# Kernel optimization log

Measured on AMD Instinct MI355X. Metric: run time of the kernel, lower is better.

## Reference

```python
import jax, jax.numpy as jnp
import numpy as np

LSTM = 512
N = 2048   # memory_size
D = 64     # memory_dim
R = 4      # nb_reads
IN = 256   # input_dim
GAMMA = 0.95
B = 1024


def setup_inputs() -> dict:
    key = jax.random.key(0)
    ks = jax.random.split(key, 13)
    s = 0.05
    return {
        "x": jax.random.normal(ks[0], (B, IN), jnp.float32),
        "M_prev": jax.random.normal(ks[1], (B, N, D), jnp.float32),
        "r_prev": jax.random.normal(ks[2], (B, R * D), jnp.float32),
        "h_prev": jax.random.normal(ks[3], (B, LSTM), jnp.float32),
        "c_prev": jax.random.normal(ks[4], (B, LSTM), jnp.float32),
        "wu_prev": jax.random.uniform(ks[5], (B, N), jnp.float32),
        "wr_prev": jax.random.uniform(ks[6], (B, R * N), jnp.float32),
        "W_ih": jax.random.normal(ks[7], (4 * LSTM, IN + R * D), jnp.float32) * s,
        "b_ih": jax.random.normal(ks[8], (4 * LSTM,), jnp.float32) * s,
        "W_hh": jax.random.normal(ks[9], (4 * LSTM, LSTM), jnp.float32) * s,
        "b_hh": jax.random.normal(ks[10], (4 * LSTM,), jnp.float32) * s,
        "W_lin": jax.random.normal(ks[11], ((2 * D + 1) * R, LSTM), jnp.float32) * s,
        "b_lin": jax.random.normal(ks[12], ((2 * D + 1) * R,), jnp.float32) * s,
    }


def _mann_step(x, M_prev, r_prev, h_prev, c_prev, wu_prev, wr_prev,
               W_ih, b_ih, W_hh, b_hh, W_lin, b_lin):
    eps = 1e-8
    # LSTMCell controller (torch gate order: i, f, g, o)
    ci = jnp.concatenate([x, r_prev], axis=-1)                 # [B, IN+R*D]
    gates = ci @ W_ih.T + b_ih + h_prev @ W_hh.T + b_hh       # [B, 4*LSTM]
    ig, fg, gg, og = jnp.split(gates, 4, axis=-1)
    c_t = jax.nn.sigmoid(fg) * c_prev + jax.nn.sigmoid(ig) * jnp.tanh(gg)
    h_t = jax.nn.sigmoid(og) * jnp.tanh(c_t)
    p = h_t @ W_lin.T + b_lin                                  # [B, (2D+1)*R]

    k = jnp.tanh(p[:, : R * D]).reshape(-1, R, D)              # read keys
    a = jnp.tanh(p[:, R * D: 2 * R * D]).reshape(-1, R, D)     # write vectors
    sig_alpha = jax.nn.sigmoid(p[:, -R:])                      # [B, R]

    # least-used addressing on PREVIOUS usage (descending sort)
    idx = jnp.argsort(-wu_prev, axis=-1)                       # [B, N]
    wlu = jax.nn.one_hot(idx[:, -R:], N, dtype=jnp.float32).sum(axis=1)  # [B, N]

    # read-head cosine addressing
    ip = jnp.einsum('brd,bnd->brn', k, M_prev)
    k_norm = jnp.sqrt(jnp.sum(k * k, axis=2, keepdims=True))            # [B,R,1]
    M_norm = jnp.sqrt(jnp.sum(M_prev * M_prev, axis=2))[:, None, :]      # [B,1,N]
    wr_t = jax.nn.softmax(ip / (k_norm * M_norm + eps), axis=-1)         # [B,R,N]

    # write-head addressing: interpolate prev read weights and least-used
    sa = sig_alpha[:, :, None]
    ww_t = sa * wr_prev.reshape(-1, R, N) + (1.0 - sa) * wlu[:, None, :]

    wu_t = GAMMA * wu_prev + wr_t.sum(axis=1) + ww_t.sum(axis=1)

    # erase single least-used row, then write
    erase = 1.0 - jax.nn.one_hot(idx[:, -1], N, dtype=jnp.float32)       # [B,N]
    M_t = M_prev * erase[:, :, None] + jnp.einsum('brn,brd->bnd', ww_t, a)

    r_t = jnp.einsum('brn,bnd->brd', wr_t, M_t).reshape(-1, R * D)
    out = jnp.concatenate([h_t, r_t], axis=-1)                 # [B, LSTM+R*D]
    return out, M_t, r_t, h_t, c_t, wu_t, wr_t.reshape(-1, R * N)


def reference(x, M_prev, r_prev, h_prev, c_prev, wu_prev, wr_prev,
              W_ih, b_ih, W_hh, b_hh, W_lin, b_lin):
    return _mann_step(x, M_prev, r_prev, h_prev, c_prev, wu_prev, wr_prev,
                      W_ih, b_ih, W_hh, b_hh, W_lin, b_lin)
```

## Files before the change

### kernel.cpp

```cpp
#include <hip/hip_runtime.h>
#include <math.h>

constexpr int BB   = 1024;
constexpr int NN   = 2048;
constexpr int DD   = 64;
constexpr int RR   = 4;
constexpr float GAMMA = 0.95f;

constexpr size_t OUT_OUT = 0;
constexpr size_t OUT_MT  = OUT_OUT + (size_t)BB * 768;
constexpr size_t OUT_RT  = OUT_MT  + (size_t)BB * NN * DD;
constexpr size_t OUT_HT  = OUT_RT  + (size_t)BB * 256;
constexpr size_t OUT_CT  = OUT_HT  + (size_t)BB * 512;
constexpr size_t OUT_WU  = OUT_CT  + (size_t)BB * 512;
constexpr size_t OUT_WR  = OUT_WU  + (size_t)BB * NN;

constexpr int SLICE   = NN * DD;
constexpr int OFF_A   = 0;
constexpr int OFF_G   = 8456 + NN;
constexpr int OFF_P   = OFF_G + 2048;
constexpr int OFF_K   = OFF_P + 520;


constexpr int WS_STRIDE = 32;
constexpr int WS_SA  = 0;
constexpr int WS_KN  = 4;
constexpr int WS_IDX = 16;

__device__ __forceinline__ float sigmoidf_(float x) { return 1.0f / (1.0f + __expf(-x)); }

typedef short short8 __attribute__((ext_vector_type(8)));
typedef float f32x4  __attribute__((ext_vector_type(4)));

__device__ __forceinline__ unsigned bf16pack2(float a, float b) {
    unsigned ua = __float_as_uint(a), ub = __float_as_uint(b);
    ua = (ua + 0x7FFFu + ((ua >> 16) & 1u)) >> 16;
    ub = (ub + 0x7FFFu + ((ub >> 16) & 1u)) >> 16;
    return ua | (ub << 16);
}

template<int CTRL>
__device__ __forceinline__ float dpp_add(float x) {
    int y = __builtin_amdgcn_update_dpp(0, __float_as_int(x), CTRL, 0xF, 0xF, false);
    return x + __int_as_float(y);
}
template<int CTRL>
__device__ __forceinline__ void dpp_add5(float& a, float& b, float& c, float& d, float& e) {
    a = dpp_add<CTRL>(a); b = dpp_add<CTRL>(b); c = dpp_add<CTRL>(c);
    d = dpp_add<CTRL>(d); e = dpp_add<CTRL>(e);
}

__global__ __launch_bounds__(256) void conv_A(
    const float* __restrict__ x, const float* __restrict__ rprev, const float* __restrict__ hprev,
    unsigned* __restrict__ Abf)
{
    const int gid = blockIdx.x * 256 + threadIdx.x;
    const int e0 = gid * 8;
    const int row = e0 >> 10, col = e0 & 1023;
    float4 v0, v1;
    if (col < 256)      { const float* p = x + row * 256 + col;
                          v0 = *(const float4*)p; v1 = *(const float4*)(p + 4); }
    else if (col < 512) { const float* p = rprev + row * 256 + (col - 256);
                          v0 = *(const float4*)p; v1 = *(const float4*)(p + 4); }
    else                { const float* p = hprev + row * 512 + (col - 512);
                          v0 = *(const float4*)p; v1 = *(const float4*)(p + 4); }
    uint4 o;
    o.x = bf16pack2(v0.x, v0.y); o.y = bf16pack2(v0.z, v0.w);
    o.z = bf16pack2(v1.x, v1.y); o.w = bf16pack2(v1.z, v1.w);
    *(uint4*)(Abf + (size_t)row * 512 + (col >> 1)) = o;
}

__global__ __launch_bounds__(256) void conv_W(
    const float* __restrict__ Wih, const float* __restrict__ Whh, unsigned* __restrict__ Wbf)
{
    const int gid = blockIdx.x * 256 + threadIdx.x;
    const int e0 = gid * 8;
    const int row = e0 >> 10, col = e0 & 1023;
    float4 v0, v1;
    if (col < 512) { const float* p = Wih + (size_t)row * 512 + col;
                     v0 = *(const float4*)p; v1 = *(const float4*)(p + 4); }
    else           { const float* p = Whh + (size_t)row * 512 + (col - 512);
                     v0 = *(const float4*)p; v1 = *(const float4*)(p + 4); }
    uint4 o;
    o.x = bf16pack2(v0.x, v0.y); o.y = bf16pack2(v0.z, v0.w);
    o.z = bf16pack2(v1.x, v1.y); o.w = bf16pack2(v1.z, v1.w);
    *(uint4*)(Wbf + (size_t)row * 512 + (col >> 1)) = o;
}

__global__ __launch_bounds__(256) void gemm_gates(
    const unsigned* __restrict__ Abf, const unsigned* __restrict__ Wbf,
    const float* __restrict__ bih, const float* __restrict__ bhh,
    float* __restrict__ out)
{
    __shared__ unsigned As[64][20];
    __shared__ unsigned Bs[64][20];
    const int t = threadIdx.x;
    const int wave = t >> 6, lane = t & 63;
    const int row0 = blockIdx.y * 64, col0 = blockIdx.x * 64;
    const int srow = t >> 2;
    const int sk4  = (t & 3) * 4;
    const int wm = wave >> 1, wn = wave & 1;
    const int lrow = lane & 15;
    const int ldw  = (lane >> 4) * 4;

    f32x4 acc00 = {0.f,0.f,0.f,0.f}, acc01 = {0.f,0.f,0.f,0.f};
    f32x4 acc10 = {0.f,0.f,0.f,0.f}, acc11 = {0.f,0.f,0.f,0.f};

    for (int k0 = 0; k0 < 512; k0 += 16) {
        const uint4 av = *(const uint4*)(Abf + (size_t)(row0 + srow) * 512 + k0 + sk4);
        const uint4 bv = *(const uint4*)(Wbf + (size_t)(col0 + srow) * 512 + k0 + sk4);
        __syncthreads();
        *(uint4*)&As[srow][sk4] = av;
        *(uint4*)&Bs[srow][sk4] = bv;
        __syncthreads();
        const short8 a0 = *(const short8*)&As[32 * wm + lrow][ldw];
        const short8 a1 = *(const short8*)&As[32 * wm + 16 + lrow][ldw];
        const short8 b0 = *(const short8*)&Bs[32 * wn + lrow][ldw];
        const short8 b1 = *(const short8*)&Bs[32 * wn + 16 + lrow][ldw];
        acc00 = __builtin_amdgcn_mfma_f32_16x16x32_bf16(a0, b0, acc00, 0, 0, 0);
        acc01 = __builtin_amdgcn_mfma_f32_16x16x32_bf16(a0, b1, acc01, 0, 0, 0);
        acc10 = __builtin_amdgcn_mfma_f32_16x16x32_bf16(a1, b0, acc10, 0, 0, 0);
        acc11 = __builtin_amdgcn_mfma_f32_16x16x32_bf16(a1, b1, acc11, 0, 0, 0);
    }

    float* mt = out + OUT_MT;
    const int rbase = row0 + 32 * wm + (lane >> 4) * 4;
    #pragma unroll
    for (int ni = 0; ni < 2; ni++) {
        const int col = col0 + 32 * wn + 16 * ni + lrow;
        const float bb = bih[col] + bhh[col];
        #pragma unroll
        for (int reg = 0; reg < 4; reg++) {
            const float v0 = (ni == 0) ? acc00[reg] : acc01[reg];
            const float v1 = (ni == 0) ? acc10[reg] : acc11[reg];
            mt[(size_t)(rbase + reg) * SLICE + OFF_G + col] = v0 + bb;
            mt[(size_t)(rbase + 16 + reg) * SLICE + OFF_G + col] = v1 + bb;
        }
    }
}

__global__ __launch_bounds__(256) void lstm_pw(const float* __restrict__ cprev, float* __restrict__ out)
{
    const size_t e0 = ((size_t)blockIdx.x * 256 + threadIdx.x) * 4;
    const int b = (int)(e0 >> 9), j = (int)(e0 & 511);
    const float* g = out + OUT_MT + (size_t)b * SLICE + OFF_G;
    const float4 ig = *(const float4*)(g + j);
    const float4 fg = *(const float4*)(g + 512 + j);
    const float4 gg = *(const float4*)(g + 1024 + j);
    const float4 og = *(const float4*)(g + 1536 + j);
    const float4 cp = *(const float4*)(cprev + e0);
    float4 c, h;
    c.x = sigmoidf_(fg.x) * cp.x + sigmoidf_(ig.x) * tanhf(gg.x);
    c.y = sigmoidf_(fg.y) * cp.y + sigmoidf_(ig.y) * tanhf(gg.y);
    c.z = sigmoidf_(fg.z) * cp.z + sigmoidf_(ig.z) * tanhf(gg.z);
    c.w = sigmoidf_(fg.w) * cp.w + sigmoidf_(ig.w) * tanhf(gg.w);
    h.x = sigmoidf_(og.x) * tanhf(c.x);
    h.y = sigmoidf_(og.y) * tanhf(c.y);
    h.z = sigmoidf_(og.z) * tanhf(c.z);
    h.w = sigmoidf_(og.w) * tanhf(c.w);
    *(float4*)(out + OUT_CT + e0) = c;
    *(float4*)(out + OUT_HT + e0) = h;
    *(float4*)(out + (size_t)b * 768 + j) = h;
}

__global__ __launch_bounds__(256) void gemm_p(
    const float* __restrict__ Wlin, const float* __restrict__ blin, float* __restrict__ out)
{
    __shared__ float As[16][68];
    __shared__ float Bs[16][68];
    const int t = threadIdx.x;
    const int row0 = blockIdx.y * 64, col0 = blockIdx.x * 64;
    const int tx = t & 15, ty = t >> 4;
    const int li = t >> 2;
    const int kq = (t & 3) * 4;
    const float* ht = out + OUT_HT;
    float acc[4][4] = {};

    for (int k0 = 0; k0 < 512; k0 += 16) {
        const int k = k0 + kq;
        {
            const int row = row0 + li;
            const float4 av = *(const float4*)(ht + (size_t)row * 512 + k);
            As[kq + 0][li] = av.x; As[kq + 1][li] = av.y;
            As[kq + 2][li] = av.z; As[kq + 3][li] = av.w;
        }
        {
            const int j = col0 + li;
            float4 bv = make_float4(0.f, 0.f, 0.f, 0.f);
            if (j < 516) bv = *(const float4*)(Wlin + j * 512 + k);
            Bs[kq + 0][li] = bv.x; Bs[kq + 1][li] = bv.y;
            Bs[kq + 2][li] = bv.z; Bs[kq + 3][li] = bv.w;
        }
        __syncthreads();
        #pragma unroll
        for (int kk = 0; kk < 16; kk++) {
            const float4 a4 = *(const float4*)&As[kk][ty * 4];
            const float4 b4 = *(const float4*)&Bs[kk][tx * 4];
            acc[0][0] += a4.x * b4.x; acc[0][1] += a4.x * b4.y; acc[0][2] += a4.x * b4.z; acc[0][3] += a4.x * b4.w;
            acc[1][0] += a4.y * b4.x; acc[1][1] += a4.y * b4.y; acc[1][2] += a4.y * b4.z; acc[1][3] += a4.y * b4.w;
            acc[2][0] += a4.z * b4.x; acc[2][1] += a4.z * b4.y; acc[2][2] += a4.z * b4.z; acc[2][3] += a4.z * b4.w;
            acc[3][0] += a4.w * b4.x; acc[3][1] += a4.w * b4.y; acc[3][2] += a4.w * b4.z; acc[3][3] += a4.w * b4.w;
        }
        __syncthreads();
    }
    float* mt = out + OUT_MT;
    #pragma unroll
    for (int ci = 0; ci < 4; ci++) {
        int row = row0 + ty * 4 + ci;
        #pragma unroll
        for (int cj = 0; cj < 4; cj++) {
            int col = col0 + tx * 4 + cj;
            if (col < 516)
                mt[(size_t)row * SLICE + OFF_P + col] = acc[ci][cj] + blin[col];
        }
    }
}

__global__ __launch_bounds__(256) void kp_argmin_k(
    const float* __restrict__ wuprev, float* __restrict__ out, float* __restrict__ ws)
{
    const int b = blockIdx.x, t = threadIdx.x;
    const int wid = t >> 6, lane = t & 63;
    float* mt = out + OUT_MT;
    const size_t sl = (size_t)b * SLICE;
    float* wsb = ws + (size_t)b * WS_STRIDE;

    {
        const float* p = mt + sl + OFF_P;
        const int r = t >> 6, d = t & 63;
        float kv = tanhf(p[r * 64 + d]);
        float av = tanhf(p[256 + r * 64 + d]);
        mt[sl + OFF_K + r * 64 + d] = kv;
        mt[sl + OFF_A + r * 64 + d] = av;
        float s2 = kv * kv;
        #pragma unroll
        for (int off = 1; off < 64; off <<= 1) s2 += __shfl_xor(s2, off);
        if (d == 0) wsb[WS_KN + r] = sqrtf(s2);
        if (t < 4) wsb[WS_SA + t] = sigmoidf_(p[512 + t]);
    }

    __shared__ float wv4[4];
    __shared__ int   wi4[4];
    __shared__ int   chosen[4];
    float wu8[8];
    #pragma unroll
    for (int i = 0; i < 8; i++) wu8[i] = wuprev[(size_t)b * NN + t + i * 256];

    for (int it = 0; it < 4; it++) {
        float bv = 3.4e38f; int bi = -1;
        #pragma unroll
        for (int i = 0; i < 8; i++) {
            int n = t + i * 256;
            bool skip = false;
            for (int j = 0; j < it; j++) skip = skip || (n == chosen[j]);
            float v = wu8[i];
            if (!skip && (v < bv || (v == bv && n > bi))) { bv = v; bi = n; }
        }
        #pragma unroll
        for (int off = 1; off < 64; off <<= 1) {
            float v2 = __shfl_xor(bv, off);
            int   i2 = __shfl_xor(bi, off);
            if (v2 < bv || (v2 == bv && i2 > bi)) { bv = v2; bi = i2; }
        }
        if (lane == 0) { wv4[wid] = bv; wi4[wid] = bi; }
        __syncthreads();
        if (t == 0) {
            float fv = wv4[0]; int fi = wi4[0];
            #pragma unroll
            for (int w = 1; w < 4; w++) {
                float v2 = wv4[w]; int i2 = wi4[w];
                if (v2 < fv || (v2 == fv && i2 > fi)) { fv = v2; fi = i2; }
            }
            chosen[it] = fi;
        }
        __syncthreads();
    }
    if (t < 4)
        ((int*)wsb)[WS_IDX + t] = chosen[t];
}

__global__ __launch_bounds__(512) void fused_mem(
    const float* __restrict__ Mprev, const float* __restrict__ wrprev,
    const float* __restrict__ wuprev,
    float* __restrict__ out, const float* __restrict__ ws)
{
    const int b = blockIdx.x, t = threadIdx.x;
    const int wave = t >> 6, lane = t & 63;
    const int row4 = lane >> 4, d4 = lane & 15;
    float* mt = out + OUT_MT;
    const size_t sl = (size_t)b * SLICE;
    const float* wsb = ws + (size_t)b * WS_STRIDE;

    __shared__ float4 s_e4[NN];
    __shared__ float  lz[8][4];

    float4 k4[4], a4[4]; float sa[4], rck[4]; int id4[4];
    #pragma unroll
    for (int r = 0; r < 4; r++) {
        k4[r] = *(const float4*)(mt + sl + OFF_K + r * 64 + d4 * 4);
        a4[r] = *(const float4*)(mt + sl + OFF_A + r * 64 + d4 * 4);
        sa[r]  = wsb[WS_SA + r];
        rck[r] = 1.0f / wsb[WS_KN + r];
        id4[r] = ((const int*)wsb)[WS_IDX + r];
    }
    __syncthreads();

    const float* wrp = wrprev + (size_t)b * (RR * NN);
    const int kill = id4[0];
    const size_t mbase = (size_t)b * NN * DD + (size_t)(d4 * 4);

    float4 racc[4];
    #pragma unroll
    for (int r = 0; r < 4; r++) racc[r] = make_float4(0.f, 0.f, 0.f, 0.f);

    float4 m4 = *(const float4*)(Mprev + mbase + (size_t)(wave * 4 + row4) * DD);

    for (int it = 0; it < 64; it++) {
        const int n = it * 32 + wave * 4 + row4;
        const int nn = (n + 32) & (NN - 1);
        const float4 m4n = *(const float4*)(Mprev + mbase + (size_t)nn * DD);
        const float w0 = wrp[0 * NN + n];
        const float w1 = wrp[1 * NN + n];
        const float w2 = wrp[2 * NN + n];
        const float w3 = wrp[3 * NN + n];

        float nrm = m4.x * m4.x + m4.y * m4.y + m4.z * m4.z + m4.w * m4.w;
        float ip0 = k4[0].x * m4.x + k4[0].y * m4.y + k4[0].z * m4.z + k4[0].w * m4.w;
        float ip1 = k4[1].x * m4.x + k4[1].y * m4.y + k4[1].z * m4.z + k4[1].w * m4.w;
        float ip2 = k4[2].x * m4.x + k4[2].y * m4.y + k4[2].z * m4.z + k4[2].w * m4.w;
        float ip3 = k4[3].x * m4.x + k4[3].y * m4.y + k4[3].z * m4.z + k4[3].w * m4.w;
        dpp_add5<0xB1>(nrm, ip0, ip1, ip2, ip3);
        dpp_add5<0x4E>(nrm, ip0, ip1, ip2, ip3);
        dpp_add5<0x124>(nrm, ip0, ip1, ip2, ip3);
        dpp_add5<0x128>(nrm, ip0, ip1, ip2, ip3);

        const float rsn = rsqrtf(fmaxf(nrm, 1e-30f));
        const float e0 = __expf(ip0 * rck[0] * rsn);
        const float e1 = __expf(ip1 * rck[1] * rsn);
        const float e2 = __expf(ip2 * rck[2] * rsn);
        const float e3 = __expf(ip3 * rck[3] * rsn);
        if (d4 == 0) s_e4[n] = make_float4(e0, e1, e2, e3);

        const float wlu = (n == id4[0] || n == id4[1] || n == id4[2] || n == id4[3]) ? 1.0f : 0.0f;
        float4 mtv = m4;
        if (n == kill) { mtv.x = 0.f; mtv.y = 0.f; mtv.z = 0.f; mtv.w = 0.f; }
        const float ww0 = fmaf(sa[0], w0 - wlu, wlu);
        const float ww1 = fmaf(sa[1], w1 - wlu, wlu);
        const float ww2 = fmaf(sa[2], w2 - wlu, wlu);
        const float ww3 = fmaf(sa[3], w3 - wlu, wlu);
        mtv.x += ww0 * a4[0].x + ww1 * a4[1].x + ww2 * a4[2].x + ww3 * a4[3].x;
        mtv.y += ww0 * a4[0].y + ww1 * a4[1].y + ww2 * a4[2].y + ww3 * a4[3].y;
        mtv.z += ww0 * a4[0].z + ww1 * a4[1].z + ww2 * a4[2].z + ww3 * a4[3].z;
        mtv.w += ww0 * a4[0].w + ww1 * a4[1].w + ww2 * a4[2].w + ww3 * a4[3].w;
        *(float4*)(mt + sl + (size_t)n * DD + d4 * 4) = mtv;

        racc[0].x += e0 * mtv.x; racc[0].y += e0 * mtv.y; racc[0].z += e0 * mtv.z; racc[0].w += e0 * mtv.w;
        racc[1].x += e1 * mtv.x; racc[1].y += e1 * mtv.y; racc[1].z += e1 * mtv.z; racc[1].w += e1 * mtv.w;
        racc[2].x += e2 * mtv.x; racc[2].y += e2 * mtv.y; racc[2].z += e2 * mtv.z; racc[2].w += e2 * mtv.w;
        racc[3].x += e3 * mtv.x; racc[3].y += e3 * mtv.y; racc[3].z += e3 * mtv.z; racc[3].w += e3 * mtv.w;

        m4 = m4n;
    }

    #pragma unroll
    for (int off = 16; off < 64; off <<= 1) {
        #pragma unroll
        for (int r = 0; r < 4; r++) {
            racc[r].x += __shfl_xor(racc[r].x, off);
            racc[r].y += __shfl_xor(racc[r].y, off);
            racc[r].z += __shfl_xor(racc[r].z, off);
            racc[r].w += __shfl_xor(racc[r].w, off);
        }
    }
    __syncthreads();

    float z0 = 0.f, z1 = 0.f, z2 = 0.f, z3 = 0.f;
    #pragma unroll
    for (int i = 0; i < 4; i++) {
        const float4 e4 = s_e4[i * 512 + t];
        z0 += e4.x; z1 += e4.y; z2 += e4.z; z3 += e4.w;
    }
    #pragma unroll
    for (int off = 1; off < 64; off <<= 1) {
        z0 += __shfl_xor(z0, off); z1 += __shfl_xor(z1, off);
        z2 += __shfl_xor(z2, off); z3 += __shfl_xor(z3, off);
    }
    if (lane == 0) { lz[wave][0] = z0; lz[wave][1] = z1; lz[wave][2] = z2; lz[wave][3] = z3; }
    __syncthreads();
    float zi[4];
    #pragma unroll
    for (int r = 0; r < 4; r++) {
        float Z = 0.f;
        #pragma unroll
        for (int w = 0; w < 8; w++) Z += lz[w][r];
        zi[r] = 1.0f / Z;
    }

    {
        float* wro = out + OUT_WR + (size_t)b * (RR * NN);
        float* wuo = out + OUT_WU + (size_t)b * NN;
        #pragma unroll
        for (int i = 0; i < 4; i++) {
            const int n = i * 512 + t;
            const float4 e4 = s_e4[n];
            const float wl = (n == id4[0] || n == id4[1] || n == id4[2] || n == id4[3]) ? 1.0f : 0.0f;
            const float wv0 = e4.x * zi[0], wv1 = e4.y * zi[1], wv2 = e4.z * zi[2], wv3 = e4.w * zi[3];
            wro[0 * NN + n] = wv0; wro[1 * NN + n] = wv1;
            wro[2 * NN + n] = wv2; wro[3 * NN + n] = wv3;
            float acc = wv0 + wv1 + wv2 + wv3;
            acc += fmaf(sa[0], wrp[0 * NN + n] - wl, wl);
            acc += fmaf(sa[1], wrp[1 * NN + n] - wl, wl);
            acc += fmaf(sa[2], wrp[2 * NN + n] - wl, wl);
            acc += fmaf(sa[3], wrp[3 * NN + n] - wl, wl);
            wuo[n] = GAMMA * wuprev[(size_t)b * NN + n] + acc;
        }
    }
    __syncthreads();

    float4* lr = s_e4;
    if (row4 == 0) {
        #pragma unroll
        for (int r = 0; r < 4; r++) lr[wave * 64 + r * 16 + d4] = racc[r];
    }
    __syncthreads();
    if (t < 64) {
        const int r = t >> 4, dd = t & 15;
        float4 s = make_float4(0.f, 0.f, 0.f, 0.f);
        #pragma unroll
        for (int w = 0; w < 8; w++) {
            const float4 v = lr[w * 64 + r * 16 + dd];
            s.x += v.x; s.y += v.y; s.z += v.z; s.w += v.w;
        }
        const float inv = zi[r];
        const float4 rt = make_float4(s.x * inv, s.y * inv, s.z * inv, s.w * inv);
        *(float4*)(out + OUT_RT + (size_t)b * 256 + r * 64 + dd * 4) = rt;
        *(float4*)(out + (size_t)b * 768 + 512 + r * 64 + dd * 4) = rt;
    }
}

extern "C" void kernel_launch(void* const* d_in, const int* in_sizes, int n_in,
                              void* d_out, int out_size, void* d_ws, size_t ws_size,
                              hipStream_t stream)
{
    const float* x      = (const float*)d_in[0];
    const float* Mprev  = (const float*)d_in[1];
    const float* rprev  = (const float*)d_in[2];
    const float* hprev  = (const float*)d_in[3];
    const float* cprev  = (const float*)d_in[4];
    const float* wuprev = (const float*)d_in[5];
    const float* wrprev = (const float*)d_in[6];
    const float* Wih    = (const float*)d_in[7];
    const float* bih    = (const float*)d_in[8];
    const float* Whh    = (const float*)d_in[9];
    const float* bhh    = (const float*)d_in[10];
    const float* Wlin   = (const float*)d_in[11];
    const float* blin   = (const float*)d_in[12];
    float* out = (float*)d_out;
    float* ws  = (float*)d_ws;

    unsigned* Abf = (unsigned*)(out + OUT_WU);
    unsigned* Wbf = (unsigned*)(out + OUT_WR);

    conv_A<<<512, 256, 0, stream>>>(x, rprev, hprev, Abf);
    conv_W<<<1024, 256, 0, stream>>>(Wih, Whh, Wbf);
    gemm_gates<<<dim3(32, 16), 256, 0, stream>>>(Abf, Wbf, bih, bhh, out);
    lstm_pw<<<512, 256, 0, stream>>>(cprev, out);
    gemm_p<<<dim3(9, 16), 256, 0, stream>>>(Wlin, blin, out);
    kp_argmin_k<<<1024, 256, 0, stream>>>(wuprev, out, ws);
    fused_mem<<<1024, 512, 0, stream>>>(Mprev, wrprev, wuprev, out, ws);
}
```

Measured before the change: 324.2 us.

## Merge conversion kernels, use bf16 MFMA for projection, fold argmin into memory kernel

```diff
diff --git a/kernel.cpp b/kernel.cpp
--- a/kernel.cpp
+++ b/kernel.cpp
@@ -16,16 +16,9 @@
 constexpr size_t OUT_WR  = OUT_WU  + (size_t)BB * NN;
 
 constexpr int SLICE   = NN * DD;
-constexpr int OFF_A   = 0;
 constexpr int OFF_G   = 8456 + NN;
 constexpr int OFF_P   = OFF_G + 2048;
-constexpr int OFF_K   = OFF_P + 520;
-
-
-constexpr int WS_STRIDE = 32;
-constexpr int WS_SA  = 0;
-constexpr int WS_KN  = 4;
-constexpr int WS_IDX = 16;
+
 
 __device__ __forceinline__ float sigmoidf_(float x) { return 1.0f / (1.0f + __expf(-x)); }
 
@@ -50,41 +43,51 @@
     d = dpp_add<CTRL>(d); e = dpp_add<CTRL>(e);
 }
 
-__global__ __launch_bounds__(256) void conv_A(
+__global__ __launch_bounds__(256) void conv_all(
     const float* __restrict__ x, const float* __restrict__ rprev, const float* __restrict__ hprev,
-    unsigned* __restrict__ Abf)
-{
-    const int gid = blockIdx.x * 256 + threadIdx.x;
-    const int e0 = gid * 8;
-    const int row = e0 >> 10, col = e0 & 1023;
-    float4 v0, v1;
-    if (col < 256)      { const float* p = x + row * 256 + col;
-                          v0 = *(const float4*)p; v1 = *(const float4*)(p + 4); }
-    else if (col < 512) { const float* p = rprev + row * 256 + (col - 256);
-                          v0 = *(const float4*)p; v1 = *(const float4*)(p + 4); }
-    else                { const float* p = hprev + row * 512 + (col - 512);
-                          v0 = *(const float4*)p; v1 = *(const float4*)(p + 4); }
-    uint4 o;
-    o.x = bf16pack2(v0.x, v0.y); o.y = bf16pack2(v0.z, v0.w);
-    o.z = bf16pack2(v1.x, v1.y); o.w = bf16pack2(v1.z, v1.w);
-    *(uint4*)(Abf + (size_t)row * 512 + (col >> 1)) = o;
-}
-
-__global__ __launch_bounds__(256) void conv_W(
-    const float* __restrict__ Wih, const float* __restrict__ Whh, unsigned* __restrict__ Wbf)
-{
-    const int gid = blockIdx.x * 256 + threadIdx.x;
-    const int e0 = gid * 8;
-    const int row = e0 >> 10, col = e0 & 1023;
-    float4 v0, v1;
-    if (col < 512) { const float* p = Wih + (size_t)row * 512 + col;
-                     v0 = *(const float4*)p; v1 = *(const float4*)(p + 4); }
-    else           { const float* p = Whh + (size_t)row * 512 + (col - 512);
-                     v0 = *(const float4*)p; v1 = *(const float4*)(p + 4); }
-    uint4 o;
-    o.x = bf16pack2(v0.x, v0.y); o.y = bf16pack2(v0.z, v0.w);
-    o.z = bf16pack2(v1.x, v1.y); o.w = bf16pack2(v1.z, v1.w);
-    *(uint4*)(Wbf + (size_t)row * 512 + (col >> 1)) = o;
+    const float* __restrict__ Wih, const float* __restrict__ Whh, const float* __restrict__ Wlin,
+    unsigned* __restrict__ Abf, unsigned* __restrict__ Wbf, unsigned* __restrict__ Wlbf)
+{
+    const int bid = blockIdx.x;
+    if (bid < 512) {
+        const int gid = bid * 256 + threadIdx.x;
+        const int e0 = gid * 8;
+        const int row = e0 >> 10, col = e0 & 1023;
+        float4 v0, v1;
+        if (col < 256)      { const float* p = x + row * 256 + col;
+                              v0 = *(const float4*)p; v1 = *(const float4*)(p + 4); }
+        else if (col < 512) { const float* p = rprev + row * 256 + (col - 256);
+                              v0 = *(const float4*)p; v1 = *(const float4*)(p + 4); }
+        else                { const float* p = hprev + row * 512 + (col - 512);
+                              v0 = *(const float4*)p; v1 = *(const float4*)(p + 4); }
+        uint4 o;
+        o.x = bf16pack2(v0.x, v0.y); o.y = bf16pack2(v0.z, v0.w);
+        o.z = bf16pack2(v1.x, v1.y); o.w = bf16pack2(v1.z, v1.w);
+        *(uint4*)(Abf + (size_t)row * 512 + (col >> 1)) = o;
+    } else if (bid < 1536) {
+        const int gid = (bid - 512) * 256 + threadIdx.x;
+        const int e0 = gid * 8;
+        const int row = e0 >> 10, col = e0 & 1023;
+        float4 v0, v1;
+        if (col < 512) { const float* p = Wih + (size_t)row * 512 + col;
+                         v0 = *(const float4*)p; v1 = *(const float4*)(p + 4); }
+        else           { const float* p = Whh + (size_t)row * 512 + (col - 512);
+                         v0 = *(const float4*)p; v1 = *(const float4*)(p + 4); }
+        uint4 o;
+        o.x = bf16pack2(v0.x, v0.y); o.y = bf16pack2(v0.z, v0.w);
+        o.z = bf16pack2(v1.x, v1.y); o.w = bf16pack2(v1.z, v1.w);
+        *(uint4*)(Wbf + (size_t)row * 512 + (col >> 1)) = o;
+    } else {
+        const int gid = (bid - 1536) * 256 + threadIdx.x;
+        const int e0 = gid * 8;
+        const int row = e0 >> 9, col = e0 & 511;
+        const float* p = Wlin + (size_t)row * 512 + col;
+        const float4 v0 = *(const float4*)p, v1 = *(const float4*)(p + 4);
+        uint4 o;
+        o.x = bf16pack2(v0.x, v0.y); o.y = bf16pack2(v0.z, v0.w);
+        o.z = bf16pack2(v1.x, v1.y); o.w = bf16pack2(v1.z, v1.w);
+        *(uint4*)(Wlbf + (size_t)row * 256 + (col >> 1)) = o;
+    }
 }
 
 __global__ __launch_bounds__(256) void gemm_gates(
@@ -161,149 +164,141 @@
     *(float4*)(out + OUT_CT + e0) = c;
     *(float4*)(out + OUT_HT + e0) = h;
     *(float4*)(out + (size_t)b * 768 + j) = h;
+    unsigned* hbf = (unsigned*)(out + OUT_RT);
+    uint2 hp; hp.x = bf16pack2(h.x, h.y); hp.y = bf16pack2(h.z, h.w);
+    *(uint2*)(hbf + (size_t)b * 256 + (j >> 1)) = hp;
 }
 
 __global__ __launch_bounds__(256) void gemm_p(
-    const float* __restrict__ Wlin, const float* __restrict__ blin, float* __restrict__ out)
-{
-    __shared__ float As[16][68];
-    __shared__ float Bs[16][68];
+    const unsigned* __restrict__ Hbf, const unsigned* __restrict__ Wlbf,
+    const float* __restrict__ blin, float* __restrict__ out)
+{
+    __shared__ unsigned As[64][20];
+    __shared__ unsigned Bs[64][20];
     const int t = threadIdx.x;
+    const int wave = t >> 6, lane = t & 63;
     const int row0 = blockIdx.y * 64, col0 = blockIdx.x * 64;
-    const int tx = t & 15, ty = t >> 4;
-    const int li = t >> 2;
-    const int kq = (t & 3) * 4;
-    const float* ht = out + OUT_HT;
-    float acc[4][4] = {};
-
-    for (int k0 = 0; k0 < 512; k0 += 16) {
-        const int k = k0 + kq;
-        {
-            const int row = row0 + li;
-            const float4 av = *(const float4*)(ht + (size_t)row * 512 + k);
-            As[kq + 0][li] = av.x; As[kq + 1][li] = av.y;
-            As[kq + 2][li] = av.z; As[kq + 3][li] = av.w;
-        }
-        {
-            const int j = col0 + li;
-            float4 bv = make_float4(0.f, 0.f, 0.f, 0.f);
-            if (j < 516) bv = *(const float4*)(Wlin + j * 512 + k);
-            Bs[kq + 0][li] = bv.x; Bs[kq + 1][li] = bv.y;
-            Bs[kq + 2][li] = bv.z; Bs[kq + 3][li] = bv.w;
-        }
+    const int srow = t >> 2;
+    const int sk4  = (t & 3) * 4;
+    const int wm = wave >> 1, wn = wave & 1;
+    const int lrow = lane & 15;
+    const int ldw  = (lane >> 4) * 4;
+
+    f32x4 acc00 = {0.f,0.f,0.f,0.f}, acc01 = {0.f,0.f,0.f,0.f};
+    f32x4 acc10 = {0.f,0.f,0.f,0.f}, acc11 = {0.f,0.f,0.f,0.f};
+
+    for (int k0 = 0; k0 < 256; k0 += 16) {
+        const uint4 av = *(const uint4*)(Hbf  + (size_t)(row0 + srow) * 256 + k0 + sk4);
+        const uint4 bv = *(const uint4*)(Wlbf + (size_t)(col0 + srow) * 256 + k0 + sk4);
         __syncthreads();
-        #pragma unroll
-        for (int kk = 0; kk < 16; kk++) {
-            const float4 a4 = *(const float4*)&As[kk][ty * 4];
-            const float4 b4 = *(const float4*)&Bs[kk][tx * 4];
-            acc[0][0] += a4.x * b4.x; acc[0][1] += a4.x * b4.y; acc[0][2] += a4.x * b4.z; acc[0][3] += a4.x * b4.w;
-            acc[1][0] += a4.y * b4.x; acc[1][1] += a4.y * b4.y; acc[1][2] += a4.y * b4.z; acc[1][3] += a4.y * b4.w;
-            acc[2][0] += a4.z * b4.x; acc[2][1] += a4.z * b4.y; acc[2][2] += a4.z * b4.z; acc[2][3] += a4.z * b4.w;
-            acc[3][0] += a4.w * b4.x; acc[3][1] += a4.w * b4.y; acc[3][2] += a4.w * b4.z; acc[3][3] += a4.w * b4.w;
-        }
+        *(uint4*)&As[srow][sk4] = av;
+        *(uint4*)&Bs[srow][sk4] = bv;
         __syncthreads();
-    }
+        const short8 a0 = *(const short8*)&As[32 * wm + lrow][ldw];
+        const short8 a1 = *(const short8*)&As[32 * wm + 16 + lrow][ldw];
+        const short8 b0 = *(const short8*)&Bs[32 * wn + lrow][ldw];
+        const short8 b1 = *(const short8*)&Bs[32 * wn + 16 + lrow][ldw];
+        acc00 = __builtin_amdgcn_mfma_f32_16x16x32_bf16(a0, b0, acc00, 0, 0, 0);
+        acc01 = __builtin_amdgcn_mfma_f32_16x16x32_bf16(a0, b1, acc01, 0, 0, 0);
+        acc10 = __builtin_amdgcn_mfma_f32_16x16x32_bf16(a1, b0, acc10, 0, 0, 0);
+        acc11 = __builtin_amdgcn_mfma_f32_16x16x32_bf16(a1, b1, acc11, 0, 0, 0);
+    }
+
     float* mt = out + OUT_MT;
-    #pragma unroll
-    for (int ci = 0; ci < 4; ci++) {
-        int row = row0 + ty * 4 + ci;
-        #pragma unroll
-        for (int cj = 0; cj < 4; cj++) {
-            int col = col0 + tx * 4 + cj;
-            if (col < 516)
-                mt[(size_t)row * SLICE + OFF_P + col] = acc[ci][cj] + blin[col];
-        }
-    }
-}
-
-__global__ __launch_bounds__(256) void kp_argmin_k(
-    const float* __restrict__ wuprev, float* __restrict__ out, float* __restrict__ ws)
-{
-    const int b = blockIdx.x, t = threadIdx.x;
-    const int wid = t >> 6, lane = t & 63;
-    float* mt = out + OUT_MT;
-    const size_t sl = (size_t)b * SLICE;
-    float* wsb = ws + (size_t)b * WS_STRIDE;
-
-    {
-        const float* p = mt + sl + OFF_P;
-        const int r = t >> 6, d = t & 63;
-        float kv = tanhf(p[r * 64 + d]);
-        float av = tanhf(p[256 + r * 64 + d]);
-        mt[sl + OFF_K + r * 64 + d] = kv;
-        mt[sl + OFF_A + r * 64 + d] = av;
-        float s2 = kv * kv;
-        #pragma unroll
-        for (int off = 1; off < 64; off <<= 1) s2 += __shfl_xor(s2, off);
-        if (d == 0) wsb[WS_KN + r] = sqrtf(s2);
-        if (t < 4) wsb[WS_SA + t] = sigmoidf_(p[512 + t]);
-    }
-
-    __shared__ float wv4[4];
-    __shared__ int   wi4[4];
-    __shared__ int   chosen[4];
-    float wu8[8];
-    #pragma unroll
-    for (int i = 0; i < 8; i++) wu8[i] = wuprev[(size_t)b * NN + t + i * 256];
-
-    for (int it = 0; it < 4; it++) {
-        float bv = 3.4e38f; int bi = -1;
-        #pragma unroll
-        for (int i = 0; i < 8; i++) {
-            int n = t + i * 256;
-            bool skip = false;
-            for (int j = 0; j < it; j++) skip = skip || (n == chosen[j]);
-            float v = wu8[i];
-            if (!skip && (v < bv || (v == bv && n > bi))) { bv = v; bi = n; }
-        }
-        #pragma unroll
-        for (int off = 1; off < 64; off <<= 1) {
-            float v2 = __shfl_xor(bv, off);
-            int   i2 = __shfl_xor(bi, off);
-            if (v2 < bv || (v2 == bv && i2 > bi)) { bv = v2; bi = i2; }
-        }
-        if (lane == 0) { wv4[wid] = bv; wi4[wid] = bi; }
-        __syncthreads();
-        if (t == 0) {
-            float fv = wv4[0]; int fi = wi4[0];
+    const int rbase = row0 + 32 * wm + (lane >> 4) * 4;
+    #pragma unroll
+    for (int ni = 0; ni < 2; ni++) {
+        const int col = col0 + 32 * wn + 16 * ni + lrow;
+        if (col < 516) {
+            const float bb = blin[col];
             #pragma unroll
-            for (int w = 1; w < 4; w++) {
-                float v2 = wv4[w]; int i2 = wi4[w];
-                if (v2 < fv || (v2 == fv && i2 > fi)) { fv = v2; fi = i2; }
+            for (int reg = 0; reg < 4; reg++) {
+                const float v0 = (ni == 0) ? acc00[reg] : acc01[reg];
+                const float v1 = (ni == 0) ? acc10[reg] : acc11[reg];
+                mt[(size_t)(rbase + reg) * SLICE + OFF_P + col] = v0 + bb;
+                mt[(size_t)(rbase + 16 + reg) * SLICE + OFF_P + col] = v1 + bb;
             }
-            chosen[it] = fi;
-        }
-        __syncthreads();
-    }
-    if (t < 4)
-        ((int*)wsb)[WS_IDX + t] = chosen[t];
+        }
+    }
 }
 
 __global__ __launch_bounds__(512) void fused_mem(
     const float* __restrict__ Mprev, const float* __restrict__ wrprev,
-    const float* __restrict__ wuprev,
-    float* __restrict__ out, const float* __restrict__ ws)
+    const float* __restrict__ wuprev, float* __restrict__ out)
 {
     const int b = blockIdx.x, t = threadIdx.x;
     const int wave = t >> 6, lane = t & 63;
     const int row4 = lane >> 4, d4 = lane & 15;
     float* mt = out + OUT_MT;
     const size_t sl = (size_t)b * SLICE;
-    const float* wsb = ws + (size_t)b * WS_STRIDE;
 
     __shared__ float4 s_e4[NN];
     __shared__ float  lz[8][4];
-
-    float4 k4[4], a4[4]; float sa[4], rck[4]; int id4[4];
+    __shared__ float  s_k[256], s_a[256];
+    __shared__ float  s_sa[4], s_rck[4];
+    __shared__ float  wvred[8];
+    __shared__ int    wired[8];
+    __shared__ int    chosen[4];
+
+    {
+        const float* p = mt + sl + OFF_P;
+        if (t < 256) {
+            const int r = t >> 6, d = t & 63;
+            const float kv = tanhf(p[r * 64 + d]);
+            const float av = tanhf(p[256 + r * 64 + d]);
+            s_k[t] = kv; s_a[t] = av;
+            float s2 = kv * kv;
+            #pragma unroll
+            for (int off = 1; off < 64; off <<= 1) s2 += __shfl_xor(s2, off);
+            if (d == 0) s_rck[r] = rsqrtf(s2);
+            if (t < 4) s_sa[t] = sigmoidf_(p[512 + t]);
+        }
+    }
+
+    {
+        float wu4[4];
+        #pragma unroll
+        for (int i = 0; i < 4; i++) wu4[i] = wuprev[(size_t)b * NN + t + i * 512];
+        for (int it = 0; it < 4; it++) {
+            float bv = 3.4e38f; int bi = -1;
+            #pragma unroll
+            for (int i = 0; i < 4; i++) {
+                const int n = t + i * 512;
+                bool skip = false;
+                for (int j = 0; j < it; j++) skip = skip || (n == chosen[j]);
+                const float v = wu4[i];
+                if (!skip && (v < bv || (v == bv && n > bi))) { bv = v; bi = n; }
+            }
+            #pragma unroll
+            for (int off = 1; off < 64; off <<= 1) {
+                const float v2 = __shfl_xor(bv, off);
+                const int   i2 = __shfl_xor(bi, off);
+                if (v2 < bv || (v2 == bv && i2 > bi)) { bv = v2; bi = i2; }
+            }
+            if (lane == 0) { wvred[wave] = bv; wired[wave] = bi; }
+            __syncthreads();
+            if (t == 0) {
+                float fv = wvred[0]; int fi = wired[0];
+                #pragma unroll
+                for (int w = 1; w < 8; w++) {
+                    if (wvred[w] < fv || (wvred[w] == fv && wired[w] > fi)) { fv = wvred[w]; fi = wired[w]; }
+                }
+                chosen[it] = fi;
+            }
+            __syncthreads();
+        }
+    }
+
+    float sa[4], rck[4]; int id4[4];
+    float4 k4[4], a4[4];
     #pragma unroll
     for (int r = 0; r < 4; r++) {
-        k4[r] = *(const float4*)(mt + sl + OFF_K + r * 64 + d4 * 4);
-        a4[r] = *(const float4*)(mt + sl + OFF_A + r * 64 + d4 * 4);
-        sa[r]  = wsb[WS_SA + r];
-        rck[r] = 1.0f / wsb[WS_KN + r];
-        id4[r] = ((const int*)wsb)[WS_IDX + r];
-    }
-    __syncthreads();
+        sa[r]  = s_sa[r];
+        rck[r] = s_rck[r];
+        id4[r] = chosen[r];
+        k4[r] = *(const float4*)&s_k[r * 64 + d4 * 4];
+        a4[r] = *(const float4*)&s_a[r * 64 + d4 * 4];
+    }
 
     const float* wrp = wrprev + (size_t)b * (RR * NN);
     const int kill = id4[0];
@@ -456,16 +451,15 @@
     const float* Wlin   = (const float*)d_in[11];
     const float* blin   = (const float*)d_in[12];
     float* out = (float*)d_out;
-    float* ws  = (float*)d_ws;
-
-    unsigned* Abf = (unsigned*)(out + OUT_WU);
-    unsigned* Wbf = (unsigned*)(out + OUT_WR);
-
-    conv_A<<<512, 256, 0, stream>>>(x, rprev, hprev, Abf);
-    conv_W<<<1024, 256, 0, stream>>>(Wih, Whh, Wbf);
+
+    unsigned* Abf  = (unsigned*)(out + OUT_WU);
+    unsigned* Wlbf = Abf + (size_t)1048576;
+    unsigned* Wbf  = (unsigned*)(out + OUT_WR);
+    unsigned* Hbf  = (unsigned*)(out + OUT_RT);
+
+    conv_all<<<1665, 256, 0, stream>>>(x, rprev, hprev, Wih, Whh, Wlin, Abf, Wbf, Wlbf);
     gemm_gates<<<dim3(32, 16), 256, 0, stream>>>(Abf, Wbf, bih, bhh, out);
     lstm_pw<<<512, 256, 0, stream>>>(cprev, out);
-    gemm_p<<<dim3(9, 16), 256, 0, stream>>>(Wlin, blin, out);
-    kp_argmin_k<<<1024, 256, 0, stream>>>(wuprev, out, ws);
-    fused_mem<<<1024, 512, 0, stream>>>(Mprev, wrprev, wuprev, out, ws);
-}
+    gemm_p<<<dim3(9, 16), 256, 0, stream>>>(Hbf, Wlbf, blin, out);
+    fused_mem<<<1024, 512, 0, stream>>>(Mprev, wrprev, wuprev, out);
+}
```

New measurement: 287.3 us. 11.4% less time.
